# Optimization experiments

Measured on AMD Instinct MI355X. Metric: run time of the kernel, lower is better.

The kernel has to match this reference:

```python
import jax, jax.numpy as jnp
import numpy as np
import math

B, S, DIM = 2, 2048, 2048
N_HEADS, N_KV_HEADS = 32, 8
HEAD_DIM = DIM // N_HEADS  # 64
N_REP = N_HEADS // N_KV_HEADS  # 4
NEG_INF = -1e9


def setup_inputs() -> dict:
    key = jax.random.key(0)
    ks = jax.random.split(key, 6)
    x = jax.random.normal(ks[0], (B, S, DIM), dtype=jnp.float32)
    # RoPE frequencies (standard Llama formulation)
    inv_freq = 1.0 / (10000.0 ** (np.arange(0, HEAD_DIM, 2, dtype=np.float32) / HEAD_DIM))
    t = np.arange(S, dtype=np.float32)
    freqs = np.outer(t, inv_freq)  # [S, HEAD_DIM//2]
    freqs_cos = jnp.asarray(np.cos(freqs), dtype=jnp.float32)
    freqs_sin = jnp.asarray(np.sin(freqs), dtype=jnp.float32)
    # additive causal mask [S, S]
    mask = jnp.where(jnp.tril(jnp.ones((S, S), dtype=bool)), 0.0, NEG_INF).astype(jnp.float32)
    sc = 1.0 / math.sqrt(DIM)
    wq = jax.random.normal(ks[1], (DIM, N_HEADS * HEAD_DIM), dtype=jnp.float32) * sc
    wk = jax.random.normal(ks[2], (DIM, N_KV_HEADS * HEAD_DIM), dtype=jnp.float32) * sc
    wv = jax.random.normal(ks[3], (DIM, N_KV_HEADS * HEAD_DIM), dtype=jnp.float32) * sc
    wo = jax.random.normal(ks[4], (N_HEADS * HEAD_DIM, DIM), dtype=jnp.float32) * sc
    return {"x": x, "freqs_cos": freqs_cos, "freqs_sin": freqs_sin, "mask": mask,
            "wq": wq, "wk": wk, "wv": wv, "wo": wo}


def _apply_rotary(x, cos, sin):
    # x: [B, S, H, HEAD_DIM]; cos/sin: [S, HEAD_DIM//2]
    b, s, h, d = x.shape
    xr = x.astype(jnp.float32).reshape(b, s, h, d // 2, 2)
    xe, xo = xr[..., 0], xr[..., 1]
    c = cos[None, :, None, :]
    sn = sin[None, :, None, :]
    oe = xe * c - xo * sn
    oo = xe * sn + xo * c
    out = jnp.stack([oe, oo], axis=-1).reshape(b, s, h, d)
    return out.astype(x.dtype)


def reference(x, freqs_cos, freqs_sin, mask, wq, wk, wv, wo):
    b, s, _ = x.shape
    xq = (x @ wq).reshape(b, s, N_HEADS, HEAD_DIM)
    xk = (x @ wk).reshape(b, s, N_KV_HEADS, HEAD_DIM)
    xv = (x @ wv).reshape(b, s, N_KV_HEADS, HEAD_DIM)
    xq = _apply_rotary(xq, freqs_cos, freqs_sin)
    xk = _apply_rotary(xk, freqs_cos, freqs_sin)
    # repeat_kv: [B, S, KVH, D] -> [B, S, H, D]
    keys = jnp.repeat(xk, N_REP, axis=2)
    values = jnp.repeat(xv, N_REP, axis=2)
    # [B, H, Q, K] scores (naive, materialized as in source)
    scores = jnp.einsum('bqhd,bkhd->bhqk', xq, keys) / math.sqrt(HEAD_DIM)
    scores = scores + mask[None, None, :, :]
    probs = jax.nn.softmax(scores.astype(jnp.float32), axis=-1).astype(xq.dtype)
    out = jnp.einsum('bhqk,bkhd->bqhd', probs, values).reshape(b, s, N_HEADS * HEAD_DIM)
    return out @ wo
```

## Files before the change

### kernel.cpp

```cpp
#include <hip/hip_runtime.h>
#include <hip/hip_bf16.h>

typedef __bf16 bf16x8 __attribute__((ext_vector_type(8)));
typedef float f32x4 __attribute__((ext_vector_type(4)));
typedef float f32x16 __attribute__((ext_vector_type(16)));
typedef short s16x4 __attribute__((ext_vector_type(4)));
typedef short s16x8 __attribute__((ext_vector_type(8)));

__device__ __forceinline__ short f2bf(float f) {
  union { __bf16 h; short s; } p; p.h = (__bf16)f; return p.s;
}
__device__ __forceinline__ float bf2f(short s) {
  union { unsigned u; float f; } v; v.u = ((unsigned)(unsigned short)s) << 16;
  return v.f;
}
__device__ __forceinline__ void gload16(const void* g, void* l) {
  __builtin_amdgcn_global_load_lds(
      (const __attribute__((address_space(1))) unsigned*)g,
      (__attribute__((address_space(3))) unsigned*)l, 16, 0, 0);
}
__device__ __forceinline__ unsigned pack2(float lo, float hi) {
  union { __bf16 h[2]; unsigned u; } p;
  p.h[0] = (__bf16)lo; p.h[1] = (__bf16)hi;
  return p.u;
}
__device__ __forceinline__ float vsum16(const f32x16& v) {
  const float a0 = v[0] + v[1], a1 = v[2] + v[3], a2 = v[4] + v[5], a3 = v[6] + v[7];
  const float a4 = v[8] + v[9], a5 = v[10] + v[11], a6 = v[12] + v[13], a7 = v[14] + v[15];
  return ((a0 + a1) + (a2 + a3)) + ((a4 + a5) + (a6 + a7));
}

constexpr float KSC = 0.18033688f;

__global__ __launch_bounds__(256) void prep_kernel(const float* __restrict__ x,
                                                   const float* __restrict__ wq,
                                                   const float* __restrict__ wk,
                                                   const float* __restrict__ wv,
                                                   const float* __restrict__ wo,
                                                   short* __restrict__ xb,
                                                   short* __restrict__ wqT,
                                                   short* __restrict__ wkT,
                                                   short* __restrict__ wvT,
                                                   short* __restrict__ woT) {
  __shared__ float T[32][33];
  const int z = blockIdx.z;
  if (z == 4) {
    const int bid = blockIdx.y * 64 + blockIdx.x;
    const int i0 = bid * 512 + threadIdx.x;
    #pragma unroll
    for (int q = 0; q < 2; ++q) {
      const int i = i0 + q * 256;
      const float4 v = reinterpret_cast<const float4*>(x)[i];
      s16x4 o;
      o[0] = f2bf(v.x); o[1] = f2bf(v.y); o[2] = f2bf(v.z); o[3] = f2bf(v.w);
      reinterpret_cast<s16x4*>(xb)[i] = o;
    }
    return;
  }
  const float* W; short* WT; int N;
  if (z == 0)      { W = wq; WT = wqT; N = 2048; }
  else if (z == 1) { W = wk; WT = wkT; N = 512; }
  else if (z == 2) { W = wv; WT = wvT; N = 512; }
  else             { W = wo; WT = woT; N = 2048; }
  const int k0 = blockIdx.x * 32, n0 = blockIdx.y * 32;
  if (n0 >= N) return;
  const int r = threadIdx.x >> 5, c = threadIdx.x & 31;
  #pragma unroll
  for (int q = 0; q < 4; ++q) T[r + q * 8][c] = W[(size_t)(k0 + r + q * 8) * N + n0 + c];
  __syncthreads();
  #pragma unroll
  for (int q = 0; q < 4; ++q)
    WT[(size_t)(n0 + r + q * 8) * 2048 + k0 + c] = f2bf(T[c][r + q * 8]);
}

__device__ __forceinline__ void rope_apply(short* __restrict__ X, const float* __restrict__ cosT,
                                           const float* __restrict__ sinT, int i, int shift,
                                           float scale) {
  const int s = (i >> shift) & 2047;
  const int p0 = (i & 7) * 4;
  s16x8 v = *reinterpret_cast<const s16x8*>(&X[(size_t)i * 8]);
  #pragma unroll
  for (int jj = 0; jj < 4; ++jj) {
    const float c = cosT[s * 32 + p0 + jj];
    const float sn = sinT[s * 32 + p0 + jj];
    const float e = bf2f(v[2 * jj]), o = bf2f(v[2 * jj + 1]);
    v[2 * jj] = f2bf((e * c - o * sn) * scale);
    v[2 * jj + 1] = f2bf((e * sn + o * c) * scale);
  }
  *reinterpret_cast<s16x8*>(&X[(size_t)i * 8]) = v;
}

__global__ void rope_both(short* __restrict__ Q, short* __restrict__ K,
                          const float* __restrict__ cosT, const float* __restrict__ sinT) {
  const int i = blockIdx.x * blockDim.x + threadIdx.x;
  if (i < 1048576) rope_apply(Q, cosT, sinT, i, 8, KSC);
  else             rope_apply(K, cosT, sinT, i - 1048576, 6, 1.0f);
}

template <int BM, int EPI>
__global__ __launch_bounds__(512, 2) void gemm256(const short* __restrict__ A,
                                                  const short* __restrict__ BT,
                                                  void* __restrict__ C0,
                                                  void* __restrict__ C1,
                                                  void* __restrict__ C2,
                                                  int M, int N, int K) {
  constexpr int BN = 256, BK = 64;
  constexpr int AIT = (BM * 8) / 512;
  constexpr int MREP = BM / 32;
  __shared__ short As[2][BM * BK];
  __shared__ short Bs[2][BN * BK];
  const int tid = threadIdx.x, lane = tid & 63, wid = tid >> 6;
  const int wm = wid >> 2, wn = wid & 3;
  const int lr = lane & 15, hi2 = lane >> 4;

  const int nwg = gridDim.x * gridDim.y;
  int bid = blockIdx.y * gridDim.x + blockIdx.x;
  bid = (bid & 7) * (nwg >> 3) + (bid >> 3);
  const int row0 = (bid % gridDim.x) * BM;
  const int col0 = (bid / gridDim.x) * BN;

  size_t aSrc[AIT]; int aDst[AIT];
  size_t bSrc[4];   int bDst[4];
  #pragma unroll
  for (int i = 0; i < AIT; ++i) {
    const int c = i * 512 + tid, r = c >> 3, ch = c & 7;
    aSrc[i] = (size_t)(row0 + r) * K + (ch ^ (r & 7)) * 8;
    aDst[i] = c * 8;
  }
  #pragma unroll
  for (int i = 0; i < 4; ++i) {
    const int c = i * 512 + tid, r = c >> 3, ch = c & 7;
    bSrc[i] = (size_t)(col0 + r) * K + (ch ^ (r & 7)) * 8;
    bDst[i] = c * 8;
  }

  f32x4 acc[MREP][4] = {};

  const int NT = K / BK;
  #pragma unroll
  for (int i = 0; i < AIT; ++i) gload16(&A[aSrc[i]], &As[0][aDst[i]]);
  #pragma unroll
  for (int i = 0; i < 4; ++i) gload16(&BT[bSrc[i]], &Bs[0][bDst[i]]);

  int buf = 0;
  for (int t = 0; t < NT; ++t) {
    __syncthreads();
    if (t + 1 < NT) {
      const int k1 = (t + 1) * BK;
      #pragma unroll
      for (int i = 0; i < AIT; ++i) gload16(&A[aSrc[i] + k1], &As[buf ^ 1][aDst[i]]);
      #pragma unroll
      for (int i = 0; i < 4; ++i) gload16(&BT[bSrc[i] + k1], &Bs[buf ^ 1][bDst[i]]);
    }
    #pragma unroll
    for (int ks = 0; ks < 2; ++ks) {
      const int sw = ((ks * 4 + hi2) ^ (lr & 7)) * 8;
      bf16x8 af[MREP], bfr[4];
      #pragma unroll
      for (int m = 0; m < MREP; ++m)
        af[m] = *reinterpret_cast<const bf16x8*>(
            &As[buf][(wm * (BM / 2) + m * 16 + lr) * BK + sw]);
      #pragma unroll
      for (int n = 0; n < 4; ++n)
        bfr[n] = *reinterpret_cast<const bf16x8*>(
            &Bs[buf][(wn * 64 + n * 16 + lr) * BK + sw]);
      __builtin_amdgcn_s_setprio(1);
      #pragma unroll
      for (int m = 0; m < MREP; ++m)
        #pragma unroll
        for (int n = 0; n < 4; ++n)
          acc[m][n] = __builtin_amdgcn_mfma_f32_16x16x32_bf16(af[m], bfr[n], acc[m][n], 0, 0, 0);
      __builtin_amdgcn_s_setprio(0);
    }
    buf ^= 1;
  }

  const int lc = lane & 15, lr4 = (lane >> 4) * 4;
  if constexpr (EPI == 1) {
    #pragma unroll
    for (int m = 0; m < MREP; ++m)
      #pragma unroll
      for (int n = 0; n < 4; ++n)
        #pragma unroll
        for (int i = 0; i < 4; ++i) {
          const int row = row0 + wm * (BM / 2) + m * 16 + lr4 + i;
          const int col = col0 + wn * 64 + n * 16 + lc;
          ((float*)C0)[(size_t)row * N + col] = acc[m][n][i];
        }
  } else {
    #pragma unroll
    for (int m = 0; m < MREP; ++m) {
      #pragma unroll
      for (int n = 0; n < 4; ++n) {
        const int row = row0 + wm * (BM / 2) + m * 16 + lr4;
        const int col = col0 + wn * 64 + n * 16 + lc;
        if (col0 < 2048) {
          #pragma unroll
          for (int i = 0; i < 4; ++i)
            ((short*)C0)[(size_t)(row + i) * 2048 + col] = f2bf(acc[m][n][i]);
        } else if (col0 < 2560) {
          #pragma unroll
          for (int i = 0; i < 4; ++i)
            ((short*)C1)[(size_t)(row + i) * 512 + (col - 2048)] = f2bf(acc[m][n][i]);
        } else {
          const int c2 = col - 2560;
          const int kvh = c2 >> 6, d = c2 & 63;
          const int bb = row >> 11, st = row & 2047;
          s16x4 o4;
          #pragma unroll
          for (int i = 0; i < 4; ++i) o4[i] = f2bf(acc[m][n][i]);
          *reinterpret_cast<s16x4*>(
              &((short*)C2)[((size_t)(bb * 8 + kvh) * 64 + d) * 2048 + st]) = o4;
        }
      }
    }
  }
}


template <bool MASKED>
__device__ __forceinline__ void ptile(const short* __restrict__ Ksb,
                                      const short* __restrict__ Vsb,
                                      const bf16x8 qf[4], int kb, int qrow,
                                      int l31, int hi,
                                      f32x16& o0, f32x16& o1, float& l_r) {
  f32x16 sa0 = {}, sa1 = {};
  __builtin_amdgcn_s_setprio(1);
  #pragma unroll
  for (int ds = 0; ds < 4; ++ds) {
    const int c0 = ((ds * 2 + hi) ^ (l31 & 7)) * 8;
    const bf16x8 kf0 = *reinterpret_cast<const bf16x8*>(&Ksb[l31 * 64 + c0]);
    const bf16x8 kf1 = *reinterpret_cast<const bf16x8*>(&Ksb[(32 + l31) * 64 + c0]);
    sa0 = __builtin_amdgcn_mfma_f32_32x32x16_bf16(kf0, qf[ds], sa0, 0, 0, 0);
    sa1 = __builtin_amdgcn_mfma_f32_32x32x16_bf16(kf1, qf[ds], sa1, 0, 0, 0);
  }
  __builtin_amdgcn_s_setprio(0);
  if (MASKED) {
    #pragma unroll
    for (int r = 0; r < 16; ++r) {
      const int kk = kb + (r & 3) + 8 * (r >> 2) + 4 * hi;
      if (kk > qrow) sa0[r] = -1e30f;
      if (kk + 32 > qrow) sa1[r] = -1e30f;
    }
  }
  #pragma unroll
  for (int r = 0; r < 16; ++r) {
    sa0[r] = exp2f(sa0[r]);
    sa1[r] = exp2f(sa1[r]);
  }
  l_r += vsum16(sa0) + vsum16(sa1);
  bf16x8 paf[4];
  #pragma unroll
  for (int ks = 0; ks < 4; ++ks) {
    union { unsigned w[4]; bf16x8 v; } u;
    #pragma unroll
    for (int w2 = 0; w2 < 4; ++w2) {
      const int rbase = (ks & 1) * 8 + w2 * 2;
      if (ks < 2) u.w[w2] = pack2(sa0[rbase], sa0[rbase + 1]);
      else        u.w[w2] = pack2(sa1[rbase], sa1[rbase + 1]);
    }
    paf[ks] = u.v;
  }
  __builtin_amdgcn_s_setprio(1);
  #pragma unroll
  for (int ks = 0; ks < 4; ++ks) {
    const int g0 = ((2 * ks) ^ (l31 & 7)) * 8 + hi * 4;
    const int g1 = ((2 * ks + 1) ^ (l31 & 7)) * 8 + hi * 4;
    union { s16x4 h2[2]; bf16x8 v; } a0, a1;
    a0.h2[0] = *reinterpret_cast<const s16x4*>(&Vsb[l31 * 64 + g0]);
    a0.h2[1] = *reinterpret_cast<const s16x4*>(&Vsb[l31 * 64 + g1]);
    a1.h2[0] = *reinterpret_cast<const s16x4*>(&Vsb[(32 + l31) * 64 + g0]);
    a1.h2[1] = *reinterpret_cast<const s16x4*>(&Vsb[(32 + l31) * 64 + g1]);
    o0 = __builtin_amdgcn_mfma_f32_32x32x16_bf16(a0.v, paf[ks], o0, 0, 0, 0);
    o1 = __builtin_amdgcn_mfma_f32_32x32x16_bf16(a1.v, paf[ks], o1, 0, 0, 0);
  }
  __builtin_amdgcn_s_setprio(0);
}

template <bool MA>
__device__ __forceinline__ void ptile2(const short* __restrict__ Ksb,
                                       const short* __restrict__ Vsb,
                                       const bf16x8 qfA[4], const bf16x8 qfB[4],
                                       int kb, int qrowA, int l31, int hi,
                                       f32x16& oA0, f32x16& oA1, f32x16& oB0, f32x16& oB1,
                                       float& lA, float& lB) {
  f32x16 a0 = {}, a1 = {}, b0 = {}, b1 = {};
  __builtin_amdgcn_s_setprio(1);
  #pragma unroll
  for (int ds = 0; ds < 4; ++ds) {
    const int c0 = ((ds * 2 + hi) ^ (l31 & 7)) * 8;
    const bf16x8 kf0 = *reinterpret_cast<const bf16x8*>(&Ksb[l31 * 64 + c0]);
    const bf16x8 kf1 = *reinterpret_cast<const bf16x8*>(&Ksb[(32 + l31) * 64 + c0]);
    a0 = __builtin_amdgcn_mfma_f32_32x32x16_bf16(kf0, qfA[ds], a0, 0, 0, 0);
    b0 = __builtin_amdgcn_mfma_f32_32x32x16_bf16(kf0, qfB[ds], b0, 0, 0, 0);
    a1 = __builtin_amdgcn_mfma_f32_32x32x16_bf16(kf1, qfA[ds], a1, 0, 0, 0);
    b1 = __builtin_amdgcn_mfma_f32_32x32x16_bf16(kf1, qfB[ds], b1, 0, 0, 0);
  }
  __builtin_amdgcn_s_setprio(0);
  if (MA) {
    #pragma unroll
    for (int r = 0; r < 16; ++r) {
      const int kk = kb + (r & 3) + 8 * (r >> 2) + 4 * hi;
      if (kk > qrowA) a0[r] = -1e30f;
      if (kk + 32 > qrowA) a1[r] = -1e30f;
    }
  }
  #pragma unroll
  for (int r = 0; r < 16; ++r) {
    a0[r] = exp2f(a0[r]);
    b0[r] = exp2f(b0[r]);
    a1[r] = exp2f(a1[r]);
    b1[r] = exp2f(b1[r]);
  }
  lA += vsum16(a0) + vsum16(a1);
  lB += vsum16(b0) + vsum16(b1);
  bf16x8 pafA[4], pafB[4];
  #pragma unroll
  for (int ks = 0; ks < 4; ++ks) {
    union { unsigned w[4]; bf16x8 v; } ua, ub;
    #pragma unroll
    for (int w2 = 0; w2 < 4; ++w2) {
      const int rbase = (ks & 1) * 8 + w2 * 2;
      if (ks < 2) { ua.w[w2] = pack2(a0[rbase], a0[rbase + 1]);
                    ub.w[w2] = pack2(b0[rbase], b0[rbase + 1]); }
      else        { ua.w[w2] = pack2(a1[rbase], a1[rbase + 1]);
                    ub.w[w2] = pack2(b1[rbase], b1[rbase + 1]); }
    }
    pafA[ks] = ua.v; pafB[ks] = ub.v;
  }
  __builtin_amdgcn_s_setprio(1);
  #pragma unroll
  for (int ks = 0; ks < 4; ++ks) {
    const int g0 = ((2 * ks) ^ (l31 & 7)) * 8 + hi * 4;
    const int g1 = ((2 * ks + 1) ^ (l31 & 7)) * 8 + hi * 4;
    union { s16x4 h2[2]; bf16x8 v; } v0, v1;
    v0.h2[0] = *reinterpret_cast<const s16x4*>(&Vsb[l31 * 64 + g0]);
    v0.h2[1] = *reinterpret_cast<const s16x4*>(&Vsb[l31 * 64 + g1]);
    v1.h2[0] = *reinterpret_cast<const s16x4*>(&Vsb[(32 + l31) * 64 + g0]);
    v1.h2[1] = *reinterpret_cast<const s16x4*>(&Vsb[(32 + l31) * 64 + g1]);
    oA0 = __builtin_amdgcn_mfma_f32_32x32x16_bf16(v0.v, pafA[ks], oA0, 0, 0, 0);
    oB0 = __builtin_amdgcn_mfma_f32_32x32x16_bf16(v0.v, pafB[ks], oB0, 0, 0, 0);
    oA1 = __builtin_amdgcn_mfma_f32_32x32x16_bf16(v1.v, pafA[ks], oA1, 0, 0, 0);
    oB1 = __builtin_amdgcn_mfma_f32_32x32x16_bf16(v1.v, pafB[ks], oB1, 0, 0, 0);
  }
  __builtin_amdgcn_s_setprio(0);
}

__global__ __launch_bounds__(512, 2) void attn3(const short* __restrict__ Q,
                                                const short* __restrict__ K,
                                                const short* __restrict__ VT,
                                                short* __restrict__ O) {
  constexpr int S = 2048, H = 32;
  const int pair = blockIdx.x, kvh = blockIdx.y, b = blockIdx.z;
  const int tid = threadIdx.x, lane = tid & 63, wid = tid >> 6;
  const int hg = wid & 3, rowhalf = wid >> 2;
  const int h = kvh * 4 + hg;
  const int l31 = lane & 31, hi = lane >> 5;
  const int qpA = pair, qpB = 31 - pair;
  const int q0A = qpA * 64 + rowhalf * 32, q0B = qpB * 64 + rowhalf * 32;
  const int qrowA = q0A + l31, qrowB = q0B + l31;
  const int bk = b * 8 + kvh;

  __shared__ short Ks[2][8192];
  __shared__ short Vs[2][8192];

  bf16x8 qfA[4], qfB[4];
  {
    const size_t qa = ((size_t)(b * S + qrowA) * H + h) * 64;
    const size_t qb = ((size_t)(b * S + qrowB) * H + h) * 64;
    #pragma unroll
    for (int ds = 0; ds < 4; ++ds) {
      qfA[ds] = *reinterpret_cast<const bf16x8*>(&Q[qa + ds * 16 + hi * 8]);
      qfB[ds] = *reinterpret_cast<const bf16x8*>(&Q[qb + ds * 16 + hi * 8]);
    }
  }

  f32x16 oA0 = {}, oA1 = {}, oB0 = {}, oB1 = {};
  float lA = 0.f, lB = 0.f;

  const int njt = (qpB + 2) >> 1;
  const size_t kroot = ((size_t)b * S * 8 + kvh) * 64;
  const size_t vroot = (size_t)bk * 64 * S;

  const int sr = tid >> 3, sch = tid & 7;
  const int cs8 = (sch ^ (sr & 7)) * 8;

  auto stage = [&](int j, int bufi) {
    #pragma unroll
    for (int s = 0; s < 2; ++s) {
      gload16(&K[kroot + (size_t)(j * 128 + s * 64 + sr) * 512 + cs8],
              &Ks[bufi][s * 4096 + tid * 8]);
      gload16(&VT[vroot + (size_t)sr * S + j * 128 + s * 64 + cs8],
              &Vs[bufi][s * 4096 + tid * 8]);
    }
  };

  stage(0, 0);
  __syncthreads();

  int cur = 0;
  for (int j = 0; j < njt; ++j) {
    if (j + 1 < njt) stage(j + 1, cur ^ 1);
    #pragma unroll
    for (int s = 0; s < 2; ++s) {
      const int kb = j * 128 + s * 64;
      const short* Ksb = &Ks[cur][s * 4096];
      const short* Vsb = &Vs[cur][s * 4096];
      if (kb <= q0A + 31) {
        if (kb + 63 <= q0A)
          ptile2<false>(Ksb, Vsb, qfA, qfB, kb, qrowA, l31, hi,
                        oA0, oA1, oB0, oB1, lA, lB);
        else
          ptile2<true>(Ksb, Vsb, qfA, qfB, kb, qrowA, l31, hi,
                       oA0, oA1, oB0, oB1, lA, lB);
      } else if (kb <= q0B + 31) {
        if (kb + 63 <= q0B)
          ptile<false>(Ksb, Vsb, qfB, kb, qrowB, l31, hi, oB0, oB1, lB);
        else
          ptile<true>(Ksb, Vsb, qfB, kb, qrowB, l31, hi, oB0, oB1, lB);
      }
    }
    __syncthreads();
    cur ^= 1;
  }

  lA += __shfl_xor(lA, 32, 64);
  lB += __shfl_xor(lB, 32, 64);
  {
    const float inv = 1.f / lA;
    const size_t obase = ((size_t)(b * S + qrowA) * H + h) * 64;
    #pragma unroll
    for (int g = 0; g < 4; ++g) {
      s16x4 s0v, s1v;
      #pragma unroll
      for (int i = 0; i < 4; ++i) {
        s0v[i] = f2bf(oA0[4 * g + i] * inv);
        s1v[i] = f2bf(oA1[4 * g + i] * inv);
      }
      *reinterpret_cast<s16x4*>(&O[obase + 8 * g + 4 * hi]) = s0v;
      *reinterpret_cast<s16x4*>(&O[obase + 32 + 8 * g + 4 * hi]) = s1v;
    }
  }
  {
    const float inv = 1.f / lB;
    const size_t obase = ((size_t)(b * S + qrowB) * H + h) * 64;
    #pragma unroll
    for (int g = 0; g < 4; ++g) {
      s16x4 s0v, s1v;
      #pragma unroll
      for (int i = 0; i < 4; ++i) {
        s0v[i] = f2bf(oB0[4 * g + i] * inv);
        s1v[i] = f2bf(oB1[4 * g + i] * inv);
      }
      *reinterpret_cast<s16x4*>(&O[obase + 8 * g + 4 * hi]) = s0v;
      *reinterpret_cast<s16x4*>(&O[obase + 32 + 8 * g + 4 * hi]) = s1v;
    }
  }
}

extern "C" void kernel_launch(void* const* d_in, const int* in_sizes, int n_in,
                              void* d_out, int out_size, void* d_ws, size_t ws_size,
                              hipStream_t stream) {
  const float* x  = (const float*)d_in[0];
  const float* fc = (const float*)d_in[1];
  const float* fs = (const float*)d_in[2];
  const float* wq = (const float*)d_in[4];
  const float* wk = (const float*)d_in[5];
  const float* wv = (const float*)d_in[6];
  const float* wo = (const float*)d_in[7];
  float* out = (float*)d_out;

  short* xb  = (short*)d_ws;
  short* wqT = xb  + 8388608;
  short* wkT = wqT + 4194304;
  short* wvT = wkT + 1048576;
  short* woT = wvT + 1048576;
  short* Qb  = woT + 4194304;
  short* Kb  = Qb  + 8388608;
  short* VTb = Kb  + 2097152;
  short* attb = xb;

  prep_kernel<<<dim3(64, 64, 5), 256, 0, stream>>>(x, wq, wk, wv, wo,
                                                   xb, wqT, wkT, wvT, woT);

  gemm256<256, 3><<<dim3(16, 12), 512, 0, stream>>>(xb, wqT, Qb, Kb, VTb, 4096, 3072, 2048);

  rope_both<<<5120, 256, 0, stream>>>(Qb, Kb, fc, fs);

  attn3<<<dim3(16, 8, 2), 512, 0, stream>>>(Qb, Kb, VTb, attb);

  gemm256<128, 1><<<dim3(32, 8), 512, 0, stream>>>(attb, woT, out, nullptr, nullptr, 4096, 2048, 2048);
}
```

Before: 227.2 us.

## Fuse Q rotary into attention and split attention blocks by row half

Q RoPE and its softmax scale now run on the register query fragments inside the attention kernel, and the standalone rope kernel handles only K. This removes a full read-modify-write pass over Q in global memory. The attention kernel is also split so each 256-thread block handles one row half, doubling the grid to 512 blocks. In exchange, K/V tiles are staged twice as often across blocks, and each thread issues twice as many staging loads.

```diff
diff --git a/kernel.cpp b/kernel.cpp
--- a/kernel.cpp
+++ b/kernel.cpp
@@ -73,28 +73,21 @@
     WT[(size_t)(n0 + r + q * 8) * 2048 + k0 + c] = f2bf(T[c][r + q * 8]);
 }
 
-__device__ __forceinline__ void rope_apply(short* __restrict__ X, const float* __restrict__ cosT,
-                                           const float* __restrict__ sinT, int i, int shift,
-                                           float scale) {
-  const int s = (i >> shift) & 2047;
+__global__ void rope_k(short* __restrict__ K, const float* __restrict__ cosT,
+                       const float* __restrict__ sinT) {
+  const int i = blockIdx.x * blockDim.x + threadIdx.x;
+  const int s = (i >> 6) & 2047;
   const int p0 = (i & 7) * 4;
-  s16x8 v = *reinterpret_cast<const s16x8*>(&X[(size_t)i * 8]);
+  s16x8 v = *reinterpret_cast<const s16x8*>(&K[(size_t)i * 8]);
   #pragma unroll
   for (int jj = 0; jj < 4; ++jj) {
     const float c = cosT[s * 32 + p0 + jj];
     const float sn = sinT[s * 32 + p0 + jj];
     const float e = bf2f(v[2 * jj]), o = bf2f(v[2 * jj + 1]);
-    v[2 * jj] = f2bf((e * c - o * sn) * scale);
-    v[2 * jj + 1] = f2bf((e * sn + o * c) * scale);
-  }
-  *reinterpret_cast<s16x8*>(&X[(size_t)i * 8]) = v;
-}
-
-__global__ void rope_both(short* __restrict__ Q, short* __restrict__ K,
-                          const float* __restrict__ cosT, const float* __restrict__ sinT) {
-  const int i = blockIdx.x * blockDim.x + threadIdx.x;
-  if (i < 1048576) rope_apply(Q, cosT, sinT, i, 8, KSC);
-  else             rope_apply(K, cosT, sinT, i - 1048576, 6, 1.0f);
+    v[2 * jj] = f2bf(e * c - o * sn);
+    v[2 * jj + 1] = f2bf(e * sn + o * c);
+  }
+  *reinterpret_cast<s16x8*>(&K[(size_t)i * 8]) = v;
 }
 
 template <int BM, int EPI>
@@ -218,6 +211,30 @@
 }
 
 
+__device__ __forceinline__ void rope_qfrag(bf16x8 qf[4], const float* __restrict__ cosT,
+                                           const float* __restrict__ sinT, int qrow, int hi) {
+  #pragma unroll
+  for (int ds = 0; ds < 4; ++ds) {
+    const int p0 = ds * 8 + hi * 4;
+    const float4 cv = *reinterpret_cast<const float4*>(&cosT[qrow * 32 + p0]);
+    const float4 sv = *reinterpret_cast<const float4*>(&sinT[qrow * 32 + p0]);
+    const float ca[4] = {cv.x, cv.y, cv.z, cv.w};
+    const float sa[4] = {sv.x, sv.y, sv.z, sv.w};
+    union { bf16x8 v; s16x8 s; } u; u.v = qf[ds];
+    s16x8 r;
+    #pragma unroll
+    for (int jj = 0; jj < 4; ++jj) {
+      const float c = ca[jj] * KSC;
+      const float sn = sa[jj] * KSC;
+      const float e = bf2f(u.s[2 * jj]), o = bf2f(u.s[2 * jj + 1]);
+      r[2 * jj] = f2bf(e * c - o * sn);
+      r[2 * jj + 1] = f2bf(e * sn + o * c);
+    }
+    union { s16x8 s; bf16x8 v; } w; w.s = r;
+    qf[ds] = w.v;
+  }
+}
+
 template <bool MASKED>
 __device__ __forceinline__ void ptile(const short* __restrict__ Ksb,
                                       const short* __restrict__ Vsb,
@@ -346,15 +363,17 @@
   __builtin_amdgcn_s_setprio(0);
 }
 
-__global__ __launch_bounds__(512, 2) void attn3(const short* __restrict__ Q,
+__global__ __launch_bounds__(256, 2) void attn4(const short* __restrict__ Q,
                                                 const short* __restrict__ K,
                                                 const short* __restrict__ VT,
+                                                const float* __restrict__ cosT,
+                                                const float* __restrict__ sinT,
                                                 short* __restrict__ O) {
   constexpr int S = 2048, H = 32;
-  const int pair = blockIdx.x, kvh = blockIdx.y, b = blockIdx.z;
+  const int pair = blockIdx.x, kvh = blockIdx.y;
+  const int b = blockIdx.z >> 1, rowhalf = blockIdx.z & 1;
   const int tid = threadIdx.x, lane = tid & 63, wid = tid >> 6;
-  const int hg = wid & 3, rowhalf = wid >> 2;
-  const int h = kvh * 4 + hg;
+  const int h = kvh * 4 + wid;
   const int l31 = lane & 31, hi = lane >> 5;
   const int qpA = pair, qpB = 31 - pair;
   const int q0A = qpA * 64 + rowhalf * 32, q0B = qpB * 64 + rowhalf * 32;
@@ -373,6 +392,8 @@
       qfA[ds] = *reinterpret_cast<const bf16x8*>(&Q[qa + ds * 16 + hi * 8]);
       qfB[ds] = *reinterpret_cast<const bf16x8*>(&Q[qb + ds * 16 + hi * 8]);
     }
+    rope_qfrag(qfA, cosT, sinT, qrowA, hi);
+    rope_qfrag(qfB, cosT, sinT, qrowB, hi);
   }
 
   f32x16 oA0 = {}, oA1 = {}, oB0 = {}, oB1 = {};
@@ -382,16 +403,19 @@
   const size_t kroot = ((size_t)b * S * 8 + kvh) * 64;
   const size_t vroot = (size_t)bk * 64 * S;
 
-  const int sr = tid >> 3, sch = tid & 7;
-  const int cs8 = (sch ^ (sr & 7)) * 8;
-
   auto stage = [&](int j, int bufi) {
     #pragma unroll
     for (int s = 0; s < 2; ++s) {
-      gload16(&K[kroot + (size_t)(j * 128 + s * 64 + sr) * 512 + cs8],
-              &Ks[bufi][s * 4096 + tid * 8]);
-      gload16(&VT[vroot + (size_t)sr * S + j * 128 + s * 64 + cs8],
-              &Vs[bufi][s * 4096 + tid * 8]);
+      #pragma unroll
+      for (int i = 0; i < 2; ++i) {
+        const int c = i * 256 + tid;
+        const int r = c >> 3, ch = c & 7;
+        const int cs8 = (ch ^ (r & 7)) * 8;
+        gload16(&K[kroot + (size_t)(j * 128 + s * 64 + r) * 512 + cs8],
+                &Ks[bufi][s * 4096 + c * 8]);
+        gload16(&VT[vroot + (size_t)r * S + j * 128 + s * 64 + cs8],
+                &Vs[bufi][s * 4096 + c * 8]);
+      }
     }
   };
 
@@ -485,9 +509,9 @@
 
   gemm256<256, 3><<<dim3(16, 12), 512, 0, stream>>>(xb, wqT, Qb, Kb, VTb, 4096, 3072, 2048);
 
-  rope_both<<<5120, 256, 0, stream>>>(Qb, Kb, fc, fs);
-
-  attn3<<<dim3(16, 8, 2), 512, 0, stream>>>(Qb, Kb, VTb, attb);
+  rope_k<<<1024, 256, 0, stream>>>(Kb, fc, fs);
+
+  attn4<<<dim3(16, 8, 4), 256, 0, stream>>>(Qb, Kb, VTb, fc, fs, attb);
 
   gemm256<128, 1><<<dim3(32, 8), 512, 0, stream>>>(attb, woT, out, nullptr, nullptr, 4096, 2048, 2048);
 }
```

After: 226.6 us. About the same (-0.3%).
